# Kernel optimization log

Hardware: AMD Instinct MI355X
Metric: run time of the kernel (lower is better)

Reference implementation:

```python
import jax, jax.numpy as jnp
import numpy as np

S = 4096
D_MODEL = 1024
D_INTERNAL = 4096


def setup_inputs() -> dict:
    key = jax.random.key(0)
    ks = jax.random.split(key, 12)
    s = 0.02
    return {
        "x": jax.random.normal(ks[0], (S, D_MODEL), dtype=jnp.float32),
        # projection weights stored as [d_in, d_out] so y = x @ W + b
        "Wq": jax.random.normal(ks[1], (D_MODEL, D_MODEL), dtype=jnp.float32) * s,
        "bq": jnp.zeros((D_MODEL,), dtype=jnp.float32),
        "Wk": jax.random.normal(ks[2], (D_MODEL, D_MODEL), dtype=jnp.float32) * s,
        "bk": jnp.zeros((D_MODEL,), dtype=jnp.float32),
        "Wv": jax.random.normal(ks[3], (D_MODEL, D_MODEL), dtype=jnp.float32) * s,
        "bv": jnp.zeros((D_MODEL,), dtype=jnp.float32),
        "W1": jax.random.normal(ks[4], (D_MODEL, D_INTERNAL), dtype=jnp.float32) * s,
        "b1": jnp.zeros((D_INTERNAL,), dtype=jnp.float32),
        "W2": jax.random.normal(ks[5], (D_INTERNAL, D_MODEL), dtype=jnp.float32) * s,
        "b2": jnp.zeros((D_MODEL,), dtype=jnp.float32),
    }


def reference(x, Wq, bq, Wk, bk, Wv, bv, W1, b1, W2, b2):
    # x: [S, D] (module is unbatched: k.transpose(0,1) implies 2-D input)
    d_model = x.shape[-1]
    q = x @ Wq + bq                         # [S, D]
    k = x @ Wk + bk                         # [S, D]
    v = x @ Wv + bv                         # [S, D]
    scores = (q @ k.T) / jnp.sqrt(jnp.asarray(d_model, x.dtype))  # [S, S]
    s = x.shape[0]
    causal = jnp.triu(jnp.ones((s, s), dtype=bool), k=1)           # True above diag
    scores = jnp.where(causal, jnp.asarray(-1e9, x.dtype), scores)
    attn = jax.nn.softmax(scores, axis=-1)  # [S, S]
    attended = attn @ v                     # [S, D]
    h = x + attended                        # residual 1
    ff = jax.nn.relu(h @ W1 + b1) @ W2 + b2 # 2-layer MLP
    out = h + ff                            # residual 2
    return (out, attn)
```

## Files before the change

### kernel.cpp

```cpp
#include <hip/hip_runtime.h>
#include <hip/hip_bf16.h>


typedef __attribute__((ext_vector_type(4))) float  f32x4;
typedef __attribute__((ext_vector_type(8))) short  bf16x8;
typedef __attribute__((ext_vector_type(4))) unsigned short us4;
typedef __attribute__((ext_vector_type(8))) unsigned short us8;

#define DEVINL __device__ __forceinline__

static constexpr int S   = 4096;
static constexpr int DM  = 1024;
static constexpr int DI  = 4096;

DEVINL unsigned short f2bf(float f) {
  union { float f; unsigned u; } v; v.f = f;
  unsigned r = v.u + 0x7fffu + ((v.u >> 16) & 1u);
  return (unsigned short)(r >> 16);
}

DEVINL void gld_lds16(const unsigned short* g, unsigned short* l) {
  __builtin_amdgcn_global_load_lds(
      (const __attribute__((address_space(1))) void*)g,
      (__attribute__((address_space(3))) void*)l,
      16, 0, 0);
}

__global__ void cvt_f32_bf16(const float* __restrict__ in,
                             unsigned short* __restrict__ out, long n) {
  long i = ((long)blockIdx.x * 256 + threadIdx.x) * 8;
  if (i >= n) return;
  f32x4 a = *(const f32x4*)(in + i);
  f32x4 b = *(const f32x4*)(in + i + 4);
  us8 o;
  o[0] = f2bf(a[0]); o[1] = f2bf(a[1]); o[2] = f2bf(a[2]); o[3] = f2bf(a[3]);
  o[4] = f2bf(b[0]); o[5] = f2bf(b[1]); o[6] = f2bf(b[2]); o[7] = f2bf(b[3]);
  *(us8*)(out + i) = o;
}

__global__ void transpose_cvt(const float* __restrict__ in,
                              unsigned short* __restrict__ out, int R, int C) {
  __shared__ float tile[32][33];
  const int bx = blockIdx.x * 32, by = blockIdx.y * 32;
  const int tx = threadIdx.x, ty = threadIdx.y;
  #pragma unroll
  for (int j = 0; j < 4; ++j) {
    int r = ty + j * 8;
    tile[r][tx] = in[(size_t)(by + r) * C + bx + tx];
  }
  __syncthreads();
  #pragma unroll
  for (int j = 0; j < 4; ++j) {
    int r = ty + j * 8;
    out[(size_t)(bx + r) * R + by + tx] = f2bf(tile[tx][r]);
  }
}

__global__ void transpose_bf16(const unsigned short* __restrict__ in, int ld,
                               unsigned short* __restrict__ out, int ldo) {
  __shared__ unsigned short tile[32][33];
  const int bx = blockIdx.x * 32, by = blockIdx.y * 32;
  const int tx = threadIdx.x, ty = threadIdx.y;
  #pragma unroll
  for (int j = 0; j < 4; ++j) {
    int r = ty + j * 8;
    tile[r][tx] = in[(size_t)(by + r) * ld + bx + tx];
  }
  __syncthreads();
  #pragma unroll
  for (int j = 0; j < 4; ++j) {
    int r = ty + j * 8;
    out[(size_t)(bx + r) * ldo + by + tx] = tile[tx][r];
  }
}

enum { EPI_QKV = 0, EPI_SC = 2, EPI_FF1 = 4, EPI_PART = 6 };

template <int EPI, bool TRI_PACK, bool TRI_TRUNC>
__launch_bounds__(512, 2)
__global__ void gemm8(const unsigned short* __restrict__ A,
                      const unsigned short* __restrict__ Bt,
                      int M, int N, int K, int lda, int ldb, int kChunk,
                      const float* __restrict__ bias,
                      float* __restrict__ Cf,
                      unsigned short* __restrict__ Cb,
                      float scale) {
  int bm, bn;
  if (TRI_PACK) {
    int t = blockIdx.x;
    bm = (int)((sqrtf(8.f * (float)t + 1.f) - 1.f) * 0.5f);
    while ((bm + 1) * (bm + 2) / 2 <= t) ++bm;
    while (bm * (bm + 1) / 2 > t) --bm;
    bn = t - bm * (bm + 1) / 2;
  } else { bm = blockIdx.y; bn = blockIdx.x; }
  const int bm0 = bm * 256, bn0 = bn * 256;

  const int kbeg = blockIdx.z * kChunk;
  int kend = min(K, kbeg + kChunk);
  if (TRI_TRUNC) kend = min(kend, bm0 + 256);
  const int NT = (kend - kbeg) >> 5;

  __shared__ __align__(16) unsigned short lds[4 * 16384];

  const int tid  = threadIdx.x;
  const int lane = tid & 63;
  const int w    = tid >> 6;
  const int wr   = w >> 2, wc = w & 3;
  const int fr   = lane & 15, fq = lane >> 4;

  f32x4 acc[8][4] = {};

  const int tq = tid >> 2;
  const int swcolE = ((tid & 3) * 8) ^ ((tq & 6) << 2);
  const unsigned short* gA0 = A  + (size_t)(bm0 + tq)       * lda + kbeg + swcolE;
  const unsigned short* gA1 = A  + (size_t)(bm0 + 128 + tq) * lda + kbeg + swcolE;
  const unsigned short* gB0 = Bt + (size_t)(bn0 + tq)       * ldb + kbeg + swcolE;
  const unsigned short* gB1 = Bt + (size_t)(bn0 + 128 + tq) * ldb + kbeg + swcolE;

  auto stageA = [&](int t_) {
    const int s_ = (t_ & 3) * 16384;
    gld_lds16(gA0 + (size_t)t_ * 32, (unsigned short*)lds + s_ + w * 512);
    gld_lds16(gA1 + (size_t)t_ * 32, (unsigned short*)lds + s_ + 4096 + w * 512);
  };
  auto stageB = [&](int t_) {
    const int s_ = (t_ & 3) * 16384;
    gld_lds16(gB0 + (size_t)t_ * 32, (unsigned short*)lds + s_ + 8192 + w * 512);
    gld_lds16(gB1 + (size_t)t_ * 32, (unsigned short*)lds + s_ + 12288 + w * 512);
  };

  const int aoffE = fr * 32 + ((fq * 8) ^ ((fr & 6) << 2));

  if (NT > 0) {
    stageA(0); stageB(0);
    if (NT > 1) { stageA(1); stageB(1); }
    if (NT > 2) { stageA(2); stageB(2); }
    if (NT > 2)      { asm volatile("s_waitcnt vmcnt(8)" ::: "memory"); }
    else if (NT > 1) { asm volatile("s_waitcnt vmcnt(4)" ::: "memory"); }
    else             { asm volatile("s_waitcnt vmcnt(0)" ::: "memory"); }
    __builtin_amdgcn_sched_barrier(0);
    __builtin_amdgcn_s_barrier();

    for (int t = 0; t < NT; ++t) {
      const unsigned short* sA = lds + (t & 3) * 16384;
      const unsigned short* sB = sA + 8192;

      bf16x8 bfrag[4], afrag[4];
      #pragma unroll
      for (int ni = 0; ni < 4; ++ni)
        bfrag[ni] = *(const bf16x8*)(sB + (wc * 64 + ni * 16) * 32 + aoffE);
      #pragma unroll
      for (int mi = 0; mi < 4; ++mi)
        afrag[mi] = *(const bf16x8*)(sA + (wr * 128 + mi * 16) * 32 + aoffE);
      if (t + 3 < NT) stageA(t + 3);
      __builtin_amdgcn_s_barrier();
      __builtin_amdgcn_s_setprio(1);
      #pragma unroll
      for (int mi = 0; mi < 4; ++mi)
        #pragma unroll
        for (int ni = 0; ni < 4; ++ni)
          acc[mi][ni] = __builtin_amdgcn_mfma_f32_16x16x32_bf16(
              afrag[mi], bfrag[ni], acc[mi][ni], 0, 0, 0);
      __builtin_amdgcn_s_setprio(0);
      __builtin_amdgcn_s_barrier();

      #pragma unroll
      for (int mi = 0; mi < 4; ++mi)
        afrag[mi] = *(const bf16x8*)(sA + (wr * 128 + 64 + mi * 16) * 32 + aoffE);
      if (t + 3 < NT) {
        stageB(t + 3);
        asm volatile("s_waitcnt vmcnt(8)" ::: "memory");
      } else if (t + 2 < NT) {
        asm volatile("s_waitcnt vmcnt(4)" ::: "memory");
      } else if (t + 1 < NT) {
        asm volatile("s_waitcnt vmcnt(0)" ::: "memory");
      }
      __builtin_amdgcn_sched_barrier(0);
      __builtin_amdgcn_s_barrier();
      __builtin_amdgcn_s_setprio(1);
      #pragma unroll
      for (int mi = 0; mi < 4; ++mi)
        #pragma unroll
        for (int ni = 0; ni < 4; ++ni)
          acc[4 + mi][ni] = __builtin_amdgcn_mfma_f32_16x16x32_bf16(
              afrag[mi], bfrag[ni], acc[4 + mi][ni], 0, 0, 0);
      __builtin_amdgcn_s_setprio(0);
      __builtin_amdgcn_s_barrier();
    }
  }

  const int row0 = bm0 + wr * 128 + fq * 4;
  const int col0 = bn0 + wc * 64 + fr;
  const size_t zoff = (EPI == EPI_PART) ? (size_t)blockIdx.z * M * N : 0;
  #pragma unroll
  for (int ni = 0; ni < 4; ++ni) {
    const int col = col0 + ni * 16;
    float bval = 0.f;
    if (EPI == EPI_QKV || EPI == EPI_FF1) bval = bias[col];
    #pragma unroll
    for (int a = 0; a < 8; ++a) {
      const int rbase = row0 + (a >> 2) * 64 + (a & 3) * 16;
      #pragma unroll
      for (int j = 0; j < 4; ++j) {
        const int row = rbase + j;
        const size_t idx = zoff + (size_t)row * N + col;
        const float c = acc[a][ni][j];
        if (EPI == EPI_QKV) {
          Cb[idx] = f2bf(c + bval);
        } else if (EPI == EPI_SC) {
          Cf[idx] = c * scale;
        } else if (EPI == EPI_FF1) {
          const float r = c + bval;
          Cb[idx] = f2bf(r > 0.f ? r : 0.f);
        } else {
          Cf[idx] = c;
        }
      }
    }
  }
}

template <bool FINAL, int Z>
__global__ void reduce_k(const float* __restrict__ P,
                         const float* __restrict__ res,
                         const float* __restrict__ bias,
                         float* __restrict__ outf,
                         unsigned short* __restrict__ outb, long n) {
  long i = ((long)blockIdx.x * 256 + threadIdx.x) * 4;
  if (i >= n) return;
  f32x4 a = *(const f32x4*)(P + i);
  #pragma unroll
  for (int z = 1; z < Z; ++z) {
    f32x4 b = *(const f32x4*)(P + (size_t)z * n + i);
    #pragma unroll
    for (int j = 0; j < 4; ++j) a[j] += b[j];
  }
  f32x4 r = *(const f32x4*)(res + i);
  if (FINAL) {
    f32x4 bb = *(const f32x4*)(bias + (i & (DM - 1)));
    f32x4 o;
    #pragma unroll
    for (int j = 0; j < 4; ++j) o[j] = a[j] + r[j] + bb[j];
    *(f32x4*)(outf + i) = o;
  } else {
    f32x4 o; us4 ob;
    #pragma unroll
    for (int j = 0; j < 4; ++j) { o[j] = a[j] + r[j]; ob[j] = f2bf(o[j]); }
    *(f32x4*)(outf + i) = o;
    *(us4*)(outb + i) = ob;
  }
}

__global__ void softmax_rows(float* __restrict__ sc,
                             unsigned short* __restrict__ attnb) {
  const int m = blockIdx.x;
  const int tid = threadIdx.x;
  const int valid = m + 1;
  float* rowf = sc + (size_t)m * S;
  unsigned short* rowb = attnb + (size_t)m * S;

  f32x4 v[4];
  float lmax = -1e30f;
  #pragma unroll
  for (int i = 0; i < 4; ++i) {
    if (i * 1024 <= m) {
      const int idx = tid * 4 + i * 1024;
      v[i] = *(const f32x4*)(rowf + idx);
      #pragma unroll
      for (int j = 0; j < 4; ++j)
        if (idx + j < valid) lmax = fmaxf(lmax, v[i][j]);
    }
  }
  #pragma unroll
  for (int off = 32; off > 0; off >>= 1)
    lmax = fmaxf(lmax, __shfl_xor(lmax, off, 64));

  __shared__ float red[8];
  if ((tid & 63) == 0) red[tid >> 6] = lmax;
  __syncthreads();
  lmax = fmaxf(fmaxf(red[0], red[1]), fmaxf(red[2], red[3]));

  f32x4 e[4];
  float lsum = 0.f;
  #pragma unroll
  for (int i = 0; i < 4; ++i) {
    const int idx = tid * 4 + i * 1024;
    #pragma unroll
    for (int j = 0; j < 4; ++j) e[i][j] = 0.f;
    if (i * 1024 <= m) {
      #pragma unroll
      for (int j = 0; j < 4; ++j) {
        const float ev = (idx + j < valid) ? __expf(v[i][j] - lmax) : 0.f;
        e[i][j] = ev;
        lsum += ev;
      }
    }
  }
  #pragma unroll
  for (int off = 32; off > 0; off >>= 1)
    lsum += __shfl_xor(lsum, off, 64);
  if ((tid & 63) == 0) red[4 + (tid >> 6)] = lsum;
  __syncthreads();
  const float tsum = red[4] + red[5] + red[6] + red[7];
  const float inv = 1.0f / tsum;

  #pragma unroll
  for (int i = 0; i < 4; ++i) {
    const int idx = tid * 4 + i * 1024;
    f32x4 o; us4 ob;
    #pragma unroll
    for (int j = 0; j < 4; ++j) {
      const float t = e[i][j] * inv;
      o[j] = t;
      ob[j] = f2bf(t);
    }
    *(f32x4*)(rowf + idx) = o;
    *(us4*)(rowb + idx) = ob;
  }
}

extern "C" void kernel_launch(void* const* d_in, const int* in_sizes, int n_in,
                              void* d_out, int out_size, void* d_ws, size_t ws_size,
                              hipStream_t stream) {
  const float* x  = (const float*)d_in[0];
  const float* Wq = (const float*)d_in[1];
  const float* bq = (const float*)d_in[2];
  const float* Wk = (const float*)d_in[3];
  const float* bk = (const float*)d_in[4];
  const float* Wv = (const float*)d_in[5];
  const float* bv = (const float*)d_in[6];
  const float* W1 = (const float*)d_in[7];
  const float* b1 = (const float*)d_in[8];
  const float* W2 = (const float*)d_in[9];
  const float* b2 = (const float*)d_in[10];
  (void)in_sizes; (void)n_in; (void)out_size;

  float* outp  = (float*)d_out;
  float* attnf = (float*)d_out + (size_t)S * DM;

  const size_t MB = 1ull << 20;
  char* ws = (char*)d_ws;
  unsigned short* W2t   = (unsigned short*)(ws + 0 * MB);
  unsigned short* W1t   = (unsigned short*)(ws + 8 * MB);
  float*          h     = (float*)(ws + 16 * MB);
  unsigned short* hb    = (unsigned short*)(ws + 32 * MB);
  unsigned short* vt    = (unsigned short*)(ws + 40 * MB);
  unsigned short* attnb = (unsigned short*)(ws + 48 * MB);
  unsigned short* qkv   = (unsigned short*)(ws + 80 * MB);
  unsigned short* xb    = (unsigned short*)(ws + 104 * MB);
  unsigned short* Wqkvt = (unsigned short*)(ws + 112 * MB);
  float*          bqkv  = (float*)(ws + 118 * MB);
  unsigned short* ff1b  = (unsigned short*)(ws + 40 * MB);
  float*          Ppv   = (float*)(ws + 80 * MB);
  float*          Pff   = (float*)(ws + 72 * MB);

  const bool big = ws_size >= 145 * MB;

  cvt_f32_bf16<<<dim3((S * DM) / 2048), 256, 0, stream>>>(x, xb, (long)S * DM);
  transpose_cvt<<<dim3(DM / 32, DM / 32), dim3(32, 8), 0, stream>>>(Wq, Wqkvt, DM, DM);
  transpose_cvt<<<dim3(DM / 32, DM / 32), dim3(32, 8), 0, stream>>>(Wk, Wqkvt + (size_t)DM * DM, DM, DM);
  transpose_cvt<<<dim3(DM / 32, DM / 32), dim3(32, 8), 0, stream>>>(Wv, Wqkvt + 2 * (size_t)DM * DM, DM, DM);
  transpose_cvt<<<dim3(DI / 32, DM / 32), dim3(32, 8), 0, stream>>>(W1, W1t, DM, DI);
  transpose_cvt<<<dim3(DM / 32, DI / 32), dim3(32, 8), 0, stream>>>(W2, W2t, DI, DM);
  hipMemcpyAsync(bqkv,          bq, DM * sizeof(float), hipMemcpyDeviceToDevice, stream);
  hipMemcpyAsync(bqkv + DM,     bk, DM * sizeof(float), hipMemcpyDeviceToDevice, stream);
  hipMemcpyAsync(bqkv + 2 * DM, bv, DM * sizeof(float), hipMemcpyDeviceToDevice, stream);

  gemm8<EPI_QKV, false, false><<<dim3(3072 / 256, S / 256, 1), 512, 0, stream>>>(
      xb, Wqkvt, S, 3072, DM, DM, DM, DM, bqkv, nullptr, qkv, 1.f);
  transpose_bf16<<<dim3(DM / 32, S / 32), dim3(32, 8), 0, stream>>>(
      qkv + 2 * DM, 3072, vt, S);

  gemm8<EPI_SC, true, false><<<dim3(136, 1, 1), 512, 0, stream>>>(
      qkv, qkv + DM, S, S, DM, 3072, 3072, DM, nullptr, attnf, nullptr, 0.03125f);

  softmax_rows<<<dim3(S), 256, 0, stream>>>(attnf, attnb);

  if (big) {
    gemm8<EPI_PART, false, true><<<dim3(DM / 256, S / 256, 4), 512, 0, stream>>>(
        attnb, vt, S, DM, S, S, S, S / 4, nullptr, Ppv, nullptr, 1.f);
    reduce_k<false, 4><<<dim3((S * DM) / 1024), 256, 0, stream>>>(
        Ppv, x, nullptr, h, hb, (long)S * DM);
  } else {
    gemm8<EPI_PART, false, true><<<dim3(DM / 256, S / 256, 2), 512, 0, stream>>>(
        attnb, vt, S, DM, S, S, S, S / 2, nullptr, Ppv, nullptr, 1.f);
    reduce_k<false, 2><<<dim3((S * DM) / 1024), 256, 0, stream>>>(
        Ppv, x, nullptr, h, hb, (long)S * DM);
  }

  gemm8<EPI_FF1, false, false><<<dim3(DI / 256, S / 256, 1), 512, 0, stream>>>(
      hb, W1t, S, DI, DM, DM, DM, DM, b1, nullptr, ff1b, 1.f);

  if (big) {
    gemm8<EPI_PART, false, false><<<dim3(DM / 256, S / 256, 4), 512, 0, stream>>>(
        ff1b, W2t, S, DM, DI, DI, DI, DI / 4, nullptr, Pff, nullptr, 1.f);
    reduce_k<true, 4><<<dim3((S * DM) / 1024), 256, 0, stream>>>(
        Pff, h, b2, outp, nullptr, (long)S * DM);
  } else {
    gemm8<EPI_PART, false, false><<<dim3(DM / 256, S / 256, 2), 512, 0, stream>>>(
        ff1b, W2t, S, DM, DI, DI, DI, DI / 2, nullptr, Pff, nullptr, 1.f);
    reduce_k<true, 2><<<dim3((S * DM) / 1024), 256, 0, stream>>>(
        Pff, h, b2, outp, nullptr, (long)S * DM);
  }
}
```

Before: 286.3 us.

## Restructure GEMM main loop to double-buffered 64-wide K tiles with split B phases

The bf16 MFMA GEMM main loop now processes 64-element K steps in two 32-wide sub-stages, using a 2-deep LDS double buffer instead of a 4-stage ring of 32-wide tiles. Each warp loads all eight A fragments at once and walks B in pairs of column fragments, so every loop iteration has four MFMA phases with prefetch for the next tile issued between them. The aim is to halve the loop iteration count and the barrier overhead per unit of K while keeping global loads overlapped with compute. The trade-offs are a shallower prefetch distance, more live A registers, and a requirement that K chunks be multiples of 64. The epilogue row mapping is changed to match the new accumulator order.

```diff
diff --git a/kernel.cpp b/kernel.cpp
--- a/kernel.cpp
+++ b/kernel.cpp
@@ -75,6 +75,9 @@
 }
 
 enum { EPI_QKV = 0, EPI_SC = 2, EPI_FF1 = 4, EPI_PART = 6 };
+
+#define VM_WAIT4 asm volatile("s_waitcnt vmcnt(4)" ::: "memory")
+#define VM_WAIT0 asm volatile("s_waitcnt vmcnt(0)" ::: "memory")
 
 template <int EPI, bool TRI_PACK, bool TRI_TRUNC>
 __launch_bounds__(512, 2)
@@ -98,9 +101,10 @@
   const int kbeg = blockIdx.z * kChunk;
   int kend = min(K, kbeg + kChunk);
   if (TRI_TRUNC) kend = min(kend, bm0 + 256);
-  const int NT = (kend - kbeg) >> 5;
-
-  __shared__ __align__(16) unsigned short lds[4 * 16384];
+  const int len = kend - kbeg;
+  const int NT = (len > 0) ? (len >> 6) : 0;
+
+  __shared__ __align__(16) unsigned short lds[2 * 4 * 8192];
 
   const int tid  = threadIdx.x;
   const int lane = tid & 63;
@@ -112,78 +116,96 @@
 
   const int tq = tid >> 2;
   const int swcolE = ((tid & 3) * 8) ^ ((tq & 6) << 2);
-  const unsigned short* gA0 = A  + (size_t)(bm0 + tq)       * lda + kbeg + swcolE;
-  const unsigned short* gA1 = A  + (size_t)(bm0 + 128 + tq) * lda + kbeg + swcolE;
-  const unsigned short* gB0 = Bt + (size_t)(bn0 + tq)       * ldb + kbeg + swcolE;
-  const unsigned short* gB1 = Bt + (size_t)(bn0 + 128 + tq) * ldb + kbeg + swcolE;
-
-  auto stageA = [&](int t_) {
-    const int s_ = (t_ & 3) * 16384;
-    gld_lds16(gA0 + (size_t)t_ * 32, (unsigned short*)lds + s_ + w * 512);
-    gld_lds16(gA1 + (size_t)t_ * 32, (unsigned short*)lds + s_ + 4096 + w * 512);
+  const unsigned short* gA = A  + (size_t)(bm0 + tq) * lda + kbeg + swcolE;
+  const unsigned short* gB = Bt + (size_t)(bn0 + tq) * ldb + kbeg + swcolE;
+  const size_t aH = (size_t)128 * lda, bH = (size_t)128 * ldb;
+
+  auto dstp = [&](int buf, int part, int h) {
+    return (unsigned short*)lds + buf * 32768 + part * 8192 + h * 4096 + w * 512;
   };
-  auto stageB = [&](int t_) {
-    const int s_ = (t_ & 3) * 16384;
-    gld_lds16(gB0 + (size_t)t_ * 32, (unsigned short*)lds + s_ + 8192 + w * 512);
-    gld_lds16(gB1 + (size_t)t_ * 32, (unsigned short*)lds + s_ + 12288 + w * 512);
+  auto stA = [&](int buf, int t_, int ks) {
+    const size_t go = (size_t)t_ * 64 + ks * 32;
+    gld_lds16(gA + go,      dstp(buf, ks ? 2 : 0, 0));
+    gld_lds16(gA + aH + go, dstp(buf, ks ? 2 : 0, 1));
   };
-
-  const int aoffE = fr * 32 + ((fq * 8) ^ ((fr & 6) << 2));
+  auto stB = [&](int buf, int t_, int ks) {
+    const size_t go = (size_t)t_ * 64 + ks * 32;
+    gld_lds16(gB + go,      dstp(buf, ks ? 3 : 1, 0));
+    gld_lds16(gB + bH + go, dstp(buf, ks ? 3 : 1, 1));
+  };
+
+  const int frSw = (fq * 8) ^ ((fr & 6) << 2);
+  auto rdA = [&](int buf, int mi, int ks) {
+    return *(const bf16x8*)((const unsigned short*)lds + buf * 32768 +
+                            (ks ? 2 : 0) * 8192 + (wr * 128 + mi * 16 + fr) * 32 + frSw);
+  };
+  auto rdB = [&](int buf, int ni, int ks) {
+    return *(const bf16x8*)((const unsigned short*)lds + buf * 32768 +
+                            (ks ? 3 : 1) * 8192 + (wc * 64 + ni * 16 + fr) * 32 + frSw);
+  };
 
   if (NT > 0) {
-    stageA(0); stageB(0);
-    if (NT > 1) { stageA(1); stageB(1); }
-    if (NT > 2) { stageA(2); stageB(2); }
-    if (NT > 2)      { asm volatile("s_waitcnt vmcnt(8)" ::: "memory"); }
-    else if (NT > 1) { asm volatile("s_waitcnt vmcnt(4)" ::: "memory"); }
-    else             { asm volatile("s_waitcnt vmcnt(0)" ::: "memory"); }
-    __builtin_amdgcn_sched_barrier(0);
+    stA(0, 0, 0); stB(0, 0, 0); stA(0, 0, 1); stB(0, 0, 1);
+    VM_WAIT4;
     __builtin_amdgcn_s_barrier();
 
     for (int t = 0; t < NT; ++t) {
-      const unsigned short* sA = lds + (t & 3) * 16384;
-      const unsigned short* sB = sA + 8192;
-
-      bf16x8 bfrag[4], afrag[4];
-      #pragma unroll
-      for (int ni = 0; ni < 4; ++ni)
-        bfrag[ni] = *(const bf16x8*)(sB + (wc * 64 + ni * 16) * 32 + aoffE);
-      #pragma unroll
-      for (int mi = 0; mi < 4; ++mi)
-        afrag[mi] = *(const bf16x8*)(sA + (wr * 128 + mi * 16) * 32 + aoffE);
-      if (t + 3 < NT) stageA(t + 3);
+      const int cur = t & 1, nxt = cur ^ 1;
+      const bool pf = (t + 1 < NT);
+      bf16x8 a[8], p, q;
+
+      #pragma unroll
+      for (int mi = 0; mi < 8; ++mi) a[mi] = rdA(cur, mi, 0);
+      p = rdB(cur, 0, 0); q = rdB(cur, 1, 0);
+      if (pf) stA(nxt, t + 1, 0);
       __builtin_amdgcn_s_barrier();
       __builtin_amdgcn_s_setprio(1);
       #pragma unroll
-      for (int mi = 0; mi < 4; ++mi)
-        #pragma unroll
-        for (int ni = 0; ni < 4; ++ni)
-          acc[mi][ni] = __builtin_amdgcn_mfma_f32_16x16x32_bf16(
-              afrag[mi], bfrag[ni], acc[mi][ni], 0, 0, 0);
+      for (int mi = 0; mi < 8; ++mi) {
+        acc[mi][0] = __builtin_amdgcn_mfma_f32_16x16x32_bf16(a[mi], p, acc[mi][0], 0, 0, 0);
+        acc[mi][1] = __builtin_amdgcn_mfma_f32_16x16x32_bf16(a[mi], q, acc[mi][1], 0, 0, 0);
+      }
       __builtin_amdgcn_s_setprio(0);
       __builtin_amdgcn_s_barrier();
 
-      #pragma unroll
-      for (int mi = 0; mi < 4; ++mi)
-        afrag[mi] = *(const bf16x8*)(sA + (wr * 128 + 64 + mi * 16) * 32 + aoffE);
-      if (t + 3 < NT) {
-        stageB(t + 3);
-        asm volatile("s_waitcnt vmcnt(8)" ::: "memory");
-      } else if (t + 2 < NT) {
-        asm volatile("s_waitcnt vmcnt(4)" ::: "memory");
-      } else if (t + 1 < NT) {
-        asm volatile("s_waitcnt vmcnt(0)" ::: "memory");
-      }
-      __builtin_amdgcn_sched_barrier(0);
+      p = rdB(cur, 2, 0); q = rdB(cur, 3, 0);
+      if (pf) stB(nxt, t + 1, 0);
       __builtin_amdgcn_s_barrier();
       __builtin_amdgcn_s_setprio(1);
       #pragma unroll
-      for (int mi = 0; mi < 4; ++mi)
-        #pragma unroll
-        for (int ni = 0; ni < 4; ++ni)
-          acc[4 + mi][ni] = __builtin_amdgcn_mfma_f32_16x16x32_bf16(
-              afrag[mi], bfrag[ni], acc[4 + mi][ni], 0, 0, 0);
+      for (int mi = 0; mi < 8; ++mi) {
+        acc[mi][2] = __builtin_amdgcn_mfma_f32_16x16x32_bf16(a[mi], p, acc[mi][2], 0, 0, 0);
+        acc[mi][3] = __builtin_amdgcn_mfma_f32_16x16x32_bf16(a[mi], q, acc[mi][3], 0, 0, 0);
+      }
       __builtin_amdgcn_s_setprio(0);
+      if (pf) { VM_WAIT4; } else { VM_WAIT0; }
+      __builtin_amdgcn_s_barrier();
+
+      #pragma unroll
+      for (int mi = 0; mi < 8; ++mi) a[mi] = rdA(cur, mi, 1);
+      p = rdB(cur, 0, 1); q = rdB(cur, 1, 1);
+      if (pf) stA(nxt, t + 1, 1);
+      __builtin_amdgcn_s_barrier();
+      __builtin_amdgcn_s_setprio(1);
+      #pragma unroll
+      for (int mi = 0; mi < 8; ++mi) {
+        acc[mi][0] = __builtin_amdgcn_mfma_f32_16x16x32_bf16(a[mi], p, acc[mi][0], 0, 0, 0);
+        acc[mi][1] = __builtin_amdgcn_mfma_f32_16x16x32_bf16(a[mi], q, acc[mi][1], 0, 0, 0);
+      }
+      __builtin_amdgcn_s_setprio(0);
+      __builtin_amdgcn_s_barrier();
+
+      p = rdB(cur, 2, 1); q = rdB(cur, 3, 1);
+      if (pf) stB(nxt, t + 1, 1);
+      __builtin_amdgcn_s_barrier();
+      __builtin_amdgcn_s_setprio(1);
+      #pragma unroll
+      for (int mi = 0; mi < 8; ++mi) {
+        acc[mi][2] = __builtin_amdgcn_mfma_f32_16x16x32_bf16(a[mi], p, acc[mi][2], 0, 0, 0);
+        acc[mi][3] = __builtin_amdgcn_mfma_f32_16x16x32_bf16(a[mi], q, acc[mi][3], 0, 0, 0);
+      }
+      __builtin_amdgcn_s_setprio(0);
+      if (pf) { VM_WAIT4; }
       __builtin_amdgcn_s_barrier();
     }
   }
@@ -197,13 +219,12 @@
     float bval = 0.f;
     if (EPI == EPI_QKV || EPI == EPI_FF1) bval = bias[col];
     #pragma unroll
-    for (int a = 0; a < 8; ++a) {
-      const int rbase = row0 + (a >> 2) * 64 + (a & 3) * 16;
+    for (int mi = 0; mi < 8; ++mi) {
       #pragma unroll
       for (int j = 0; j < 4; ++j) {
-        const int row = rbase + j;
+        const int row = row0 + mi * 16 + j;
         const size_t idx = zoff + (size_t)row * N + col;
-        const float c = acc[a][ni][j];
+        const float c = acc[mi][ni][j];
         if (EPI == EPI_QKV) {
           Cb[idx] = f2bf(c + bval);
         } else if (EPI == EPI_SC) {
```

Result: no change. 289.2 us (+1.0%).
